# Optimization experiments

Hardware: AMD Instinct MI355X
Metric: run time of the kernel (lower is better)

## Reference

```python
import jax, jax.numpy as jnp
import numpy as np

# --- module hyperparameters (from init_kwargs) ---
NUM_HEADS = 16
ATTN_DIM = 1024
HEAD_DIM = ATTN_DIM // NUM_HEADS  # 64
NUM_RF = 256                      # FAVOR random features per head
CONV_CH = 1024
GROUPS = 4
M_SCALE = 256                     # num_features_per_scale
GAMMAS = (0.5, 1.0, 2.0)          # gamma_list
NY_LANDMARKS = 64                 # == HEAD_DIM so shapes compose
NY_GAMMA = 1.0
EPS = 1e-6


def setup_inputs() -> dict:
    key = jax.random.key(0)
    ks = jax.random.split(key, 12)
    B, S, C = 2, 4096, CONV_CH
    G, Ms = len(GAMMAS), M_SCALE
    x = jax.random.normal(ks[0], (B, S, C), dtype=jnp.float32)
    # grouped Conv1D kernels (WIO layout): [ksize, Cin/groups, Cout], one per q/k/v
    conv_k = jax.random.normal(ks[1], (3, 3, C // GROUPS, C), jnp.float32) / np.sqrt(3 * (C // GROUPS))
    conv_b = jnp.zeros((3, C), jnp.float32)
    # multi-scale random-Fourier-feature weights per projection and per gamma scale
    rff_w = jax.random.normal(ks[2], (3, G, C, Ms), jnp.float32)
    rff_b = jax.random.uniform(ks[3], (3, G, Ms), jnp.float32) * (2.0 * np.pi)
    proj_w = jax.random.normal(ks[4], (3, G * Ms, ATTN_DIM), jnp.float32) / np.sqrt(G * Ms)
    proj_b = jnp.zeros((3, ATTN_DIM), jnp.float32)
    # FAVOR+ projection matrix (shared across heads) and Nystrom landmarks
    omega = jax.random.normal(ks[5], (HEAD_DIM, NUM_RF), jnp.float32)
    landmarks = jax.random.normal(ks[6], (NY_LANDMARKS, HEAD_DIM), jnp.float32)
    out_w = jax.random.normal(ks[7], (ATTN_DIM, ATTN_DIM), jnp.float32) / np.sqrt(ATTN_DIM)
    out_b = jnp.zeros((ATTN_DIM,), jnp.float32)
    return {"x": x, "conv_k": conv_k, "conv_b": conv_b, "rff_w": rff_w, "rff_b": rff_b,
            "proj_w": proj_w, "proj_b": proj_b, "omega": omega, "landmarks": landmarks,
            "out_w": out_w, "out_b": out_b}


def _rotary(seq_len, dh, dtype):
    inv = 1.0 / (10000.0 ** (jnp.arange(0, dh, 2, dtype=jnp.float32) / dh))
    f = jnp.arange(seq_len, dtype=jnp.float32)[:, None] * inv[None, :]  # [S, dh/2]
    emb = jnp.concatenate([f, f], axis=-1)  # [S, dh]
    return jnp.sin(emb).astype(dtype), jnp.cos(emb).astype(dtype)


def _apply_rope(x, sin, cos):
    # x: [B,H,S,D]; rotate-half RoPE
    d = x.shape[-1] // 2
    rot = jnp.concatenate([-x[..., d:], x[..., :d]], axis=-1)
    return x * cos + rot * sin


def _projection(x, ck, cb, rw, rb, pw, pb):
    # ProjectionWithKernel: grouped conv -> multi-scale RFF kernel map -> dense
    h = jax.lax.conv_general_dilated(x, ck, (1,), 'SAME',
                                     dimension_numbers=('NWC', 'WIO', 'NWC'),
                                     feature_group_count=GROUPS) + cb
    g = jnp.sqrt(2.0 * jnp.array(GAMMAS, dtype=x.dtype))[:, None]  # [G,1]
    z = jnp.cos(jnp.einsum('bsc,gcm->bsgm', h, rw) * g + rb)       # [B,S,G,Ms]
    feats = (z * jnp.sqrt(2.0 / M_SCALE)).reshape(x.shape[0], x.shape[1], -1)
    return feats @ pw + pb  # [B,S,ATTN_DIM]


def _favor(x, omega):
    # FAVOR+ positive random features: exp(x.w - |x|^2/2) / sqrt(m)
    norm = 0.5 * jnp.sum(x * x, axis=-1, keepdims=True)
    return jnp.exp(jnp.einsum('bhsd,dm->bhsm', x, omega) - norm) / jnp.sqrt(float(omega.shape[-1]))


def _nystrom(k, landmarks):
    # RBF features against landmarks (normalized by dim to keep exp in range)
    d = k.shape[-1]
    d2 = (jnp.sum(k * k, -1, keepdims=True) + jnp.sum(landmarks * landmarks, -1)
          - 2.0 * jnp.einsum('bhsd,ld->bhsl', k, landmarks))
    return jnp.exp(-NY_GAMMA * d2 / d)  # [B,H,S,L], L == HEAD_DIM


def reference(x, conv_k, conv_b, rff_w, rff_b, proj_w, proj_b, omega, landmarks, out_w, out_b):
    B, S, _ = x.shape
    qkv = [_projection(x, conv_k[i], conv_b[i], rff_w[i], rff_b[i], proj_w[i], proj_b[i])
           for i in range(3)]
    split = lambda t: t.reshape(B, S, NUM_HEADS, HEAD_DIM).transpose(0, 2, 1, 3)
    q, k, v = map(split, qkv)  # [B,H,S,Dh]
    sin, cos = _rotary(S, HEAD_DIM, x.dtype)
    q = _apply_rope(q, sin, cos)
    k = _apply_rope(k, sin, cos)
    k = _nystrom(k, landmarks)               # [B,H,S,Dh]
    qp = _favor(q, omega)                    # [B,H,S,M]
    kp = _favor(k, omega)                    # [B,H,S,M]
    denom = jnp.einsum('bhse,bhe->bhs', qp, jnp.sum(kp, axis=2))[..., None]
    kv = jnp.einsum('bhse,bhsd->bhed', kp, v)          # [B,H,M,Dh]
    num = jnp.einsum('bhse,bhed->bhsd', qp, kv)        # [B,H,S,Dh]
    out = num / (denom + EPS)
    out = out.transpose(0, 2, 1, 3).reshape(B, S, ATTN_DIM)
    return out @ out_w + out_b  # dropout is identity at inference
```

## Files before the change

### kernel.cpp

```cpp
#include <hip/hip_runtime.h>
#include <math.h>


using f32x4 = __attribute__((ext_vector_type(4))) float;
using s16x8 = __attribute__((ext_vector_type(8))) short;

__device__ __forceinline__ unsigned short f2bf(float x) {
  unsigned u = __float_as_uint(x);
  unsigned r = u + 0x7fffu + ((u >> 16) & 1u);
  return (unsigned short)(r >> 16);
}
__device__ __forceinline__ float bf2f(unsigned short h) {
  return __uint_as_float(((unsigned)h) << 16);
}

__device__ __forceinline__ void gload16(const void* g, void* l) {
  __builtin_amdgcn_global_load_lds(
      (const __attribute__((address_space(1))) void*)g,
      (__attribute__((address_space(3))) void*)l, 16, 0, 0);
}

__global__ __launch_bounds__(256) void split_prep_kernel(
    const float* __restrict__ in, unsigned short* __restrict__ ohi,
    unsigned short* __restrict__ olo, int n8)
{
  const int i = blockIdx.x * 256 + threadIdx.x;
  if (i >= n8) return;
  const float4 f0 = ((const float4*)in)[i * 2];
  const float4 f1 = ((const float4*)in)[i * 2 + 1];
  const float v[8] = {f0.x, f0.y, f0.z, f0.w, f1.x, f1.y, f1.z, f1.w};
  s16x8 hi, lo;
  #pragma unroll
  for (int u = 0; u < 8; ++u) {
    const unsigned short hh = f2bf(v[u]);
    hi[u] = (short)hh;
    lo[u] = (short)f2bf(v[u] - bf2f(hh));
  }
  ((s16x8*)ohi)[i] = hi;
  ((s16x8*)olo)[i] = lo;
}

template<int WM>
__global__ __launch_bounds__(256) void wconv_kernel(
    const float* __restrict__ in0, unsigned short* __restrict__ ohi,
    unsigned short* __restrict__ olo)
{
  int K, N;
  const float* in;
  unsigned short *oh, *ol = nullptr;
  const int z = blockIdx.z;
  if constexpr (WM == 0) {
    K = 768; N = 1024;
    in = in0 + (size_t)z * 786432;
    oh = ohi + (size_t)z * 786432; ol = olo + (size_t)z * 786432;
  } else if constexpr (WM == 1) {
    K = 1024; N = 256;
    const int i = z / 3, g = z % 3;
    in = in0 + (size_t)i * 786432 + (size_t)g * 262144;
    oh = ohi + (size_t)i * 786432 + (size_t)g * 262144;
    ol = olo + (size_t)i * 786432 + (size_t)g * 262144;
  } else if constexpr (WM == 2) {
    K = 768; N = 1024;
    in = in0 + (size_t)z * 786432; oh = ohi + (size_t)z * 786432;
  } else {
    K = 1024; N = 1024; in = in0; oh = ohi;
  }
  const int k0 = blockIdx.x * 64, n0 = blockIdx.y * 64;
  __shared__ float t[64][65];
  const int tid = threadIdx.x, tn = tid & 63, tr = tid >> 6;
  #pragma unroll 4
  for (int p = 0; p < 16; ++p) {
    const int kk = p * 4 + tr;
    t[kk][tn] = in[(size_t)(k0 + kk) * N + n0 + tn];
  }
  __syncthreads();
  #pragma unroll 4
  for (int p = 0; p < 16; ++p) {
    const int nn = p * 4 + tr;
    const float v = t[tn][nn];
    const unsigned short hi = f2bf(v);
    oh[(size_t)(n0 + nn) * K + k0 + tn] = hi;
    if constexpr (WM <= 1)
      ol[(size_t)(n0 + nn) * K + k0 + tn] = f2bf(v - bf2f(hi));
  }
}

__global__ __launch_bounds__(256) void omega_prep_kernel(
    const float* __restrict__ omega, unsigned short* __restrict__ oThi)
{
  const int idx = blockIdx.x * 256 + threadIdx.x;
  const int m = idx >> 6, d = idx & 63;
  oThi[idx] = f2bf(omega[d * 256 + m]);
}

__global__ __launch_bounds__(256) void vt_kernel(
    const float* __restrict__ V, unsigned short* __restrict__ VT)
{
  const int bh = blockIdx.x, sb = blockIdx.y;
  const int b = bh >> 4, h = bh & 15;
  __shared__ float t[64][65];
  const int tid = threadIdx.x, tn = tid & 63, tr = tid >> 6;
  #pragma unroll 4
  for (int p = 0; p < 16; ++p)
    t[p * 4 + tr][tn] =
        V[(size_t)(b * 4096 + sb * 64 + p * 4 + tr) * 1024 + h * 64 + tn];
  __syncthreads();
  #pragma unroll 4
  for (int p = 0; p < 16; ++p)
    VT[((size_t)bh * 80 + p * 4 + tr) * 4096 + sb * 64 + tn] =
        f2bf(t[tn][p * 4 + tr]);
  #pragma unroll
  for (int p = 0; p < 4; ++p) {
    const int rr = p * 4 + tr;
    VT[((size_t)bh * 80 + 64 + rr) * 4096 + sb * 64 + tn] =
        (rr == 0) ? 0x3F80 : 0;
  }
}

template<int MODE>
__global__ __launch_bounds__(256, 4) void gemm_mfma(
    const unsigned short* __restrict__ Ahi, const unsigned short* __restrict__ Alo,
    const unsigned short* __restrict__ Bhig, const unsigned short* __restrict__ Blog,
    const float* __restrict__ bias, const float2* __restrict__ tab,
    float* __restrict__ Cf, unsigned short* __restrict__ C1,
    unsigned short* __restrict__ C2,
    int M, int N, int K)
{
  constexpr bool SPLIT = (MODE <= 1);
  __shared__ alignas(16) char smem[SPLIT ? 32768 : 16384];
  char* const sAhi = smem;
  char* const sBhi = smem + (SPLIT ? 16384 : 8192);
  char* const sAlo = smem + 8192;
  char* const sBlo = smem + 24576;

  const int gx = gridDim.x, gy = gridDim.y;
  const int L = blockIdx.x + gx * (blockIdx.y + gy * blockIdx.z);
  const int nwg = gx * gy * gridDim.z;
  const int logical = (L & 7) * (nwg >> 3) + (L >> 3);
  const int bx = logical % gx;
  const int by = (logical / gx) % gy;
  const int z = logical / (gx * gy);

  if constexpr (MODE == 0) {
    Bhig += (size_t)z * 786432; Blog += (size_t)z * 786432;
    bias += z * 1024;
    C1 += (size_t)z * 8388608; C2 += (size_t)z * 8388608;
  } else if constexpr (MODE == 1) {
    Ahi += (size_t)z * 8388608; Alo += (size_t)z * 8388608;
    Bhig += (size_t)z * 786432; Blog += (size_t)z * 786432;
    bias += z * 768;
    C1 += (size_t)z * 6291456;
  } else if constexpr (MODE == 2) {
    Ahi += (size_t)z * 6291456;
    Bhig += (size_t)z * 786432;
    bias += z * 1024;
    Cf += (size_t)z * 8388608;
  }

  const int tid = threadIdx.x;
  const int n0 = bx * 128;
  const int m0 = by * 128;

  const int lane = tid & 63, wid = tid >> 6;
  const int wr = wid >> 1, wc = wid & 1;
  const int fr = lane & 15, kc = lane >> 4;
  const int fsw = ((fr >> 1) & 3) << 4;

  const int seg0 = wid * 2;
  const int r0 = seg0 * 16 + (lane >> 2);
  const int r1 = r0 + 16;
  const int cp = lane & 3;
  const int c0e = (cp ^ ((r0 >> 1) & 3)) * 8;
  const int c1e = (cp ^ ((r1 >> 1) & 3)) * 8;
  char* const dA0 = sAhi + seg0 * 1024;  char* const dA1 = dA0 + 1024;
  char* const dL0 = sAlo + seg0 * 1024;  char* const dL1 = dL0 + 1024;
  char* const dB0 = sBhi + seg0 * 1024;  char* const dB1 = dB0 + 1024;
  char* const dBl0 = sBlo + seg0 * 1024; char* const dBl1 = dBl0 + 1024;

  f32x4 acc[4][4];
  #pragma unroll
  for (int i = 0; i < 4; ++i)
    #pragma unroll
    for (int j = 0; j < 4; ++j) acc[i][j] = f32x4{0.f, 0.f, 0.f, 0.f};

  for (int k0 = 0; k0 < K; k0 += 32) {
    __syncthreads();
    if constexpr (MODE == 0) {
      const int t = k0 >> 8;
      const int cb = (n0 >> 8) * 256 + (k0 & 255);
      const int g0 = m0 + r0, g1 = m0 + r1;
      int s0 = (g0 & 4095) + t - 1; s0 = s0 < 0 ? 0 : (s0 > 4095 ? 4095 : s0);
      int s1 = (g1 & 4095) + t - 1; s1 = s1 < 0 ? 0 : (s1 > 4095 ? 4095 : s1);
      const size_t o0 = ((size_t)((g0 >> 12) * 4096 + s0)) * 1024 + cb;
      const size_t o1 = ((size_t)((g1 >> 12) * 4096 + s1)) * 1024 + cb;
      gload16(Ahi + o0 + c0e, dA0);
      gload16(Ahi + o1 + c1e, dA1);
      gload16(Alo + o0 + c0e, dL0);
      gload16(Alo + o1 + c1e, dL1);
    } else {
      const size_t o0 = (size_t)(m0 + r0) * K + k0;
      const size_t o1 = (size_t)(m0 + r1) * K + k0;
      gload16(Ahi + o0 + c0e, dA0);
      gload16(Ahi + o1 + c1e, dA1);
      if constexpr (SPLIT) {
        gload16(Alo + o0 + c0e, dL0);
        gload16(Alo + o1 + c1e, dL1);
      }
    }
    {
      const size_t o0 = (size_t)(n0 + r0) * K + k0;
      const size_t o1 = (size_t)(n0 + r1) * K + k0;
      gload16(Bhig + o0 + c0e, dB0);
      gload16(Bhig + o1 + c1e, dB1);
      if constexpr (SPLIT) {
        gload16(Blog + o0 + c0e, dBl0);
        gload16(Blog + o1 + c1e, dBl1);
      }
    }
    __syncthreads();

    if constexpr (MODE == 0) {
      const int t = k0 >> 8;
      int zr = -1;
      if (t == 0 && (m0 & 4095) == 0) zr = 0;
      if (t == 2 && (m0 & 4095) == 3968) zr = 127;
      if (zr >= 0) {
        if (tid < 8) {
          char* buf = (tid < 4) ? sAhi : sAlo;
          *(s16x8*)(buf + zr * 64 + (tid & 3) * 16) = s16x8{0,0,0,0,0,0,0,0};
        }
        __syncthreads();
      }
    }

    s16x8 Af[4], Al[4], Bf[4], Bl[4];
    #pragma unroll
    for (int i = 0; i < 4; ++i) {
      const int off = (wr * 64 + i * 16 + fr) * 64 + ((kc * 16) ^ fsw);
      Af[i] = *(const s16x8*)(sAhi + off);
      if constexpr (SPLIT) Al[i] = *(const s16x8*)(sAlo + off);
    }
    #pragma unroll
    for (int j = 0; j < 4; ++j) {
      const int off = (wc * 64 + j * 16 + fr) * 64 + ((kc * 16) ^ fsw);
      Bf[j] = *(const s16x8*)(sBhi + off);
      if constexpr (SPLIT) Bl[j] = *(const s16x8*)(sBlo + off);
    }
    #pragma unroll
    for (int i = 0; i < 4; ++i)
      #pragma unroll
      for (int j = 0; j < 4; ++j) {
        acc[i][j] = __builtin_amdgcn_mfma_f32_16x16x32_bf16(Af[i], Bf[j], acc[i][j], 0, 0, 0);
        if constexpr (SPLIT) {
          acc[i][j] = __builtin_amdgcn_mfma_f32_16x16x32_bf16(Af[i], Bl[j], acc[i][j], 0, 0, 0);
          acc[i][j] = __builtin_amdgcn_mfma_f32_16x16x32_bf16(Al[i], Bf[j], acc[i][j], 0, 0, 0);
        }
      }
  }

  if constexpr (MODE == 2) {
    #pragma unroll
    for (int i = 0; i < 4; ++i)
      #pragma unroll
      for (int j2 = 0; j2 < 2; ++j2) {
        const int col0 = n0 + wc * 64 + j2 * 16 + fr;
        const int jr = col0 & 31;
        const float b0 = bias[col0], b1 = bias[col0 + 32];
        #pragma unroll
        for (int rr = 0; rr < 4; ++rr) {
          const int row = m0 + wr * 64 + i * 16 + kc * 4 + rr;
          float v0 = acc[i][j2][rr] + b0;
          float v1 = acc[i][j2 + 2][rr] + b1;
          if (z < 2) {
            const float2 cs = tab[((row & 4095) << 5) | jr];
            const float rr0 = v0 * cs.x - v1 * cs.y;
            const float rr1 = v1 * cs.x + v0 * cs.y;
            v0 = rr0; v1 = rr1;
          }
          Cf[(size_t)row * N + col0] = v0;
          Cf[(size_t)row * N + col0 + 32] = v1;
        }
      }
  } else {
    #pragma unroll
    for (int i = 0; i < 4; ++i)
      #pragma unroll
      for (int j = 0; j < 4; ++j) {
        const int col = n0 + wc * 64 + j * 16 + fr;
        #pragma unroll
        for (int rr = 0; rr < 4; ++rr) {
          const int row = m0 + wr * 64 + i * 16 + kc * 4 + rr;
          const float v = acc[i][j][rr];
          if constexpr (MODE == 0) {
            const float hv = v + bias[col];
            const unsigned short hh = f2bf(hv);
            C1[(size_t)row * N + col] = hh;
            C2[(size_t)row * N + col] = f2bf(hv - bf2f(hh));
          } else if constexpr (MODE == 1) {
            const int g = col >> 8;
            const float sg = (g == 0) ? 1.0f : ((g == 1) ? 1.41421356237309515f : 2.0f);
            const float zc = cosf(v * sg + bias[col]) * 0.08838834764831845f;
            C1[(size_t)row * N + col] = f2bf(zc);
          } else {
            Cf[(size_t)row * N + col] = v + bias[col];
          }
        }
      }
  }
}

__global__ __launch_bounds__(256) void rope_table_kernel(float2* __restrict__ tab)
{
  const int idx = blockIdx.x * 256 + threadIdx.x;
  const int j = idx & 31, s = idx >> 5;
  const double inv = pow(10000.0, -(double)j * (1.0 / 32.0));
  double sd, cd;
  sincos((double)s * inv, &sd, &cd);
  tab[idx] = make_float2((float)cd, (float)sd);
}

__global__ __launch_bounds__(256) void nystrom_mfma(
    const float* __restrict__ Kb, const float* __restrict__ lm,
    unsigned short* __restrict__ kny, float* __restrict__ knorm)
{
  const int bid = blockIdx.x;
  const int bh = bid >> 4, chunk = bid & 15;
  const int b = bh >> 4, h = bh & 15;
  const int tid = threadIdx.x, lane = tid & 63, wid = tid >> 6;
  const int fr = lane & 15, kc = lane >> 4;
  const int ws0 = chunk * 256 + wid * 64;

  __shared__ float lnorm[64];
  if (tid < 64) {
    float s = 0.f;
    #pragma unroll
    for (int d = 0; d < 64; ++d) { const float v = lm[tid * 64 + d]; s = fmaf(v, v, s); }
    lnorm[tid] = s;
  }
  __syncthreads();

  s16x8 bfr[4][2];
  #pragma unroll
  for (int c = 0; c < 4; ++c)
    #pragma unroll
    for (int ks = 0; ks < 2; ++ks) {
      const float* lp = lm + (c * 16 + fr) * 64 + ks * 32 + kc * 8;
      #pragma unroll
      for (int u = 0; u < 8; ++u) bfr[c][ks][u] = (short)f2bf(lp[u]);
    }

  #pragma unroll
  for (int r = 0; r < 4; ++r) {
    const int s_r = ws0 + r * 16 + fr;
    const float* ap = Kb + ((size_t)(b * 4096 + s_r)) * 1024 + h * 64;
    s16x8 afr[2];
    float part = 0.f;
    #pragma unroll
    for (int ks = 0; ks < 2; ++ks) {
      const float4 f0 = *(const float4*)(ap + ks * 32 + kc * 8);
      const float4 f1 = *(const float4*)(ap + ks * 32 + kc * 8 + 4);
      const float v[8] = {f0.x, f0.y, f0.z, f0.w, f1.x, f1.y, f1.z, f1.w};
      #pragma unroll
      for (int u = 0; u < 8; ++u) {
        part = fmaf(v[u], v[u], part);
        afr[ks][u] = (short)f2bf(v[u]);
      }
    }
    part += __shfl_xor(part, 16);
    part += __shfl_xor(part, 32);

    float sq[4] = {0.f, 0.f, 0.f, 0.f};
    #pragma unroll
    for (int c = 0; c < 4; ++c) {
      f32x4 acc = f32x4{0.f, 0.f, 0.f, 0.f};
      acc = __builtin_amdgcn_mfma_f32_16x16x32_bf16(afr[0], bfr[c][0], acc, 0, 0, 0);
      acc = __builtin_amdgcn_mfma_f32_16x16x32_bf16(afr[1], bfr[c][1], acc, 0, 0, 0);
      const float ln = lnorm[c * 16 + fr];
      #pragma unroll
      for (int reg = 0; reg < 4; ++reg) {
        const float nk = __shfl(part, kc * 4 + reg);
        const float val = __expf((2.f * acc[reg] - nk - ln) * 0.015625f);
        sq[reg] = fmaf(val, val, sq[reg]);
        const int srow = ws0 + r * 16 + kc * 4 + reg;
        kny[((size_t)(b * 4096 + srow) * 16 + h) * 64 + c * 16 + fr] = f2bf(val);
      }
    }
    #pragma unroll
    for (int reg = 0; reg < 4; ++reg) {
      float s2 = sq[reg];
      s2 += __shfl_xor(s2, 1); s2 += __shfl_xor(s2, 2);
      s2 += __shfl_xor(s2, 4); s2 += __shfl_xor(s2, 8);
      if (fr == 0) {
        const int srow = ws0 + r * 16 + kc * 4 + reg;
        knorm[(size_t)(b * 4096 + srow) * 16 + h] = 0.5f * s2;
      }
    }
  }
}

__global__ __launch_bounds__(512) void favor_k_mfma(
    const unsigned short* __restrict__ kny, const float* __restrict__ knorm,
    const unsigned short* __restrict__ oThi,
    const unsigned short* __restrict__ VT, float* __restrict__ KVp)
{
  const int bid = blockIdx.x;
  const int bh = bid >> 3, chunk = bid & 7;
  const int b = bh >> 4, h = bh & 15;
  const int s0 = chunk * 512;
  const int tid = threadIdx.x, lane = tid & 63, wid = tid >> 6;
  const int fr = lane & 15, kc = lane >> 4;
  const int m0w = wid * 32;

  __shared__ unsigned short P[256][40];
  __shared__ float T[8][32][84];

  s16x8 whi[2][2];
  #pragma unroll
  for (int c = 0; c < 2; ++c)
    #pragma unroll
    for (int ks = 0; ks < 2; ++ks)
      whi[c][ks] = *(const s16x8*)(oThi + (size_t)(m0w + c * 16 + fr) * 64 + ks * 32 + kc * 8);

  f32x4 acc2[2][5];
  #pragma unroll
  for (int i = 0; i < 2; ++i)
    #pragma unroll
    for (int j = 0; j < 5; ++j) acc2[i][j] = f32x4{0.f, 0.f, 0.f, 0.f};

  for (int st = 0; st < 512; st += 32) {
    s16x8 a1[2][2];
    float nrm[2];
    #pragma unroll
    for (int r = 0; r < 2; ++r) {
      const size_t kidx = (size_t)(b * 4096 + s0 + st + r * 16 + fr) * 16 + h;
      a1[r][0] = *(const s16x8*)(kny + kidx * 64 + kc * 8);
      a1[r][1] = *(const s16x8*)(kny + kidx * 64 + 32 + kc * 8);
      nrm[r] = knorm[kidx];
    }
    __syncthreads();
    #pragma unroll
    for (int r = 0; r < 2; ++r)
      #pragma unroll
      for (int c = 0; c < 2; ++c) {
        f32x4 s1 = f32x4{0.f, 0.f, 0.f, 0.f};
        s1 = __builtin_amdgcn_mfma_f32_16x16x32_bf16(a1[r][0], whi[c][0], s1, 0, 0, 0);
        s1 = __builtin_amdgcn_mfma_f32_16x16x32_bf16(a1[r][1], whi[c][1], s1, 0, 0, 0);
        #pragma unroll
        for (int reg = 0; reg < 4; ++reg) {
          const int sl = kc * 4 + reg;
          const float nn = __shfl(nrm[r], sl);
          const float p = __expf(s1[reg] - nn - 2.772588722239781f);
          P[m0w + c * 16 + fr][r * 16 + sl] = f2bf(p);
        }
      }
    __syncthreads();
    s16x8 b2[5];
    #pragma unroll
    for (int nf = 0; nf < 5; ++nf)
      b2[nf] = *(const s16x8*)(VT + ((size_t)bh * 80 + nf * 16 + fr) * 4096 +
                               s0 + st + kc * 8);
    #pragma unroll
    for (int mf = 0; mf < 2; ++mf) {
      const s16x8 a2 = *(const s16x8*)&P[m0w + mf * 16 + fr][kc * 8];
      #pragma unroll
      for (int nf = 0; nf < 5; ++nf)
        acc2[mf][nf] = __builtin_amdgcn_mfma_f32_16x16x32_bf16(a2, b2[nf], acc2[mf][nf], 0, 0, 0);
    }
  }
  #pragma unroll
  for (int mf = 0; mf < 2; ++mf)
    #pragma unroll
    for (int nf = 0; nf < 5; ++nf)
      #pragma unroll
      for (int reg = 0; reg < 4; ++reg)
        T[wid][mf * 16 + kc * 4 + reg][nf * 16 + fr] = acc2[mf][nf][reg];
  __syncthreads();
  #pragma unroll
  for (int i = 0; i < 40; ++i) {
    const int flat = i * 64 + lane;
    const int n = flat >> 5, ml = flat & 31;
    KVp[((size_t)bid * 80 + n) * 256 + m0w + ml] = T[wid][ml][n];
  }
}

__global__ __launch_bounds__(256) void reduce_kvxt_kernel(
    const float* __restrict__ KVp, unsigned short* __restrict__ KVXT)
{
  const int bh = blockIdx.x;
  const int m = threadIdx.x;
  for (int n = 0; n < 80; ++n) {
    float s = 0.f;
    #pragma unroll
    for (int c = 0; c < 8; ++c)
      s += KVp[((size_t)(bh * 8 + c) * 80 + n) * 256 + m];
    KVXT[((size_t)bh * 80 + n) * 256 + m] = f2bf(s);
  }
}

__global__ __launch_bounds__(512) void favor_q_mfma(
    const float* __restrict__ Q, const unsigned short* __restrict__ oThi,
    const unsigned short* __restrict__ KVXT, unsigned short* __restrict__ O)
{
  const int bid = blockIdx.x;
  const int bh = bid >> 4, chunk = bid & 15;
  const int b = bh >> 4, h = bh & 15;
  const int s0 = chunk * 256;
  const int tid = threadIdx.x, lane = tid & 63, wid = tid >> 6;
  const int fr = lane & 15, kc = lane >> 4;
  const int ws0 = s0 + wid * 32;

  __shared__ unsigned short KX[80][264];
  __shared__ unsigned short P[8][32][66];

  for (int i = tid; i < 80 * 256; i += 512)
    KX[i >> 8][i & 255] = KVXT[(size_t)bh * 80 * 256 + i];
  __syncthreads();

  s16x8 ahi[2][2];
  float nrm[2];
  #pragma unroll
  for (int r = 0; r < 2; ++r) {
    float part = 0.f;
    #pragma unroll
    for (int ks = 0; ks < 2; ++ks) {
      const float* ap = Q + ((size_t)(b * 4096 + ws0 + r * 16 + fr)) * 1024 +
                        h * 64 + ks * 32 + kc * 8;
      const float4 f0 = ((const float4*)ap)[0];
      const float4 f1 = ((const float4*)ap)[1];
      const float v[8] = {f0.x, f0.y, f0.z, f0.w, f1.x, f1.y, f1.z, f1.w};
      #pragma unroll
      for (int u = 0; u < 8; ++u) {
        part = fmaf(v[u], v[u], part);
        ahi[r][ks][u] = (short)f2bf(v[u]);
      }
    }
    part += __shfl_xor(part, 16);
    part += __shfl_xor(part, 32);
    nrm[r] = 0.5f * part;
  }

  f32x4 acc2[2][5];
  #pragma unroll
  for (int i = 0; i < 2; ++i)
    #pragma unroll
    for (int j = 0; j < 5; ++j) acc2[i][j] = f32x4{0.f, 0.f, 0.f, 0.f};

  for (int mc = 0; mc < 4; ++mc) {
    __syncthreads();
    #pragma unroll
    for (int r = 0; r < 2; ++r)
      #pragma unroll
      for (int c = 0; c < 4; ++c) {
        f32x4 s1 = f32x4{0.f, 0.f, 0.f, 0.f};
        #pragma unroll
        for (int ks = 0; ks < 2; ++ks) {
          const size_t off = (size_t)(mc * 64 + c * 16 + fr) * 64 + ks * 32 + kc * 8;
          const s16x8 bh1 = *(const s16x8*)(oThi + off);
          s1 = __builtin_amdgcn_mfma_f32_16x16x32_bf16(ahi[r][ks], bh1, s1, 0, 0, 0);
        }
        #pragma unroll
        for (int reg = 0; reg < 4; ++reg) {
          const int sl = kc * 4 + reg;
          const float nn = __shfl(nrm[r], sl);
          const float p = __expf(s1[reg] - nn - 2.772588722239781f);
          P[wid][r * 16 + sl][c * 16 + fr] = f2bf(p);
        }
      }
    __syncthreads();
    #pragma unroll
    for (int ks2 = 0; ks2 < 2; ++ks2) {
      s16x8 b2[5];
      #pragma unroll
      for (int nf = 0; nf < 5; ++nf)
        b2[nf] = *(const s16x8*)&KX[nf * 16 + fr][mc * 64 + ks2 * 32 + kc * 8];
      #pragma unroll
      for (int r = 0; r < 2; ++r) {
        const s16x8 a2 = *(const s16x8*)&P[wid][r * 16 + fr][ks2 * 32 + kc * 8];
        #pragma unroll
        for (int nf = 0; nf < 5; ++nf)
          acc2[r][nf] = __builtin_amdgcn_mfma_f32_16x16x32_bf16(a2, b2[nf], acc2[r][nf], 0, 0, 0);
      }
    }
  }
  #pragma unroll
  for (int r = 0; r < 2; ++r)
    #pragma unroll
    for (int reg = 0; reg < 4; ++reg) {
      const int s = ws0 + r * 16 + kc * 4 + reg;
      const float dv = __shfl(acc2[r][4][reg], lane & 48) + 1e-6f;
      #pragma unroll
      for (int nf = 0; nf < 4; ++nf)
        O[(size_t)(b * 4096 + s) * 1024 + h * 64 + nf * 16 + fr] =
            f2bf(acc2[r][nf][reg] / dv);
    }
}

extern "C" void kernel_launch(void* const* d_in, const int* in_sizes, int n_in,
                              void* d_out, int out_size, void* d_ws, size_t ws_size,
                              hipStream_t stream)
{
  const float* x      = (const float*)d_in[0];
  const float* conv_k = (const float*)d_in[1];
  const float* conv_b = (const float*)d_in[2];
  const float* rff_w  = (const float*)d_in[3];
  const float* rff_b  = (const float*)d_in[4];
  const float* proj_w = (const float*)d_in[5];
  const float* proj_b = (const float*)d_in[6];
  const float* omega  = (const float*)d_in[7];
  const float* lm     = (const float*)d_in[8];
  const float* out_w  = (const float*)d_in[9];
  const float* out_b  = (const float*)d_in[10];

  char* wsb = (char*)d_ws;
  size_t o = 0;
  auto alloc = [&](size_t bytes) {
    char* p = wsb + o;
    o = (o + bytes + 255) & ~(size_t)255;
    return p;
  };
  unsigned short* Wc_hi = (unsigned short*)alloc(4718592);
  unsigned short* Wc_lo = (unsigned short*)alloc(4718592);
  unsigned short* Wr_hi = (unsigned short*)alloc(4718592);
  unsigned short* Wr_lo = (unsigned short*)alloc(4718592);
  unsigned short* Wp    = (unsigned short*)alloc(4718592);
  unsigned short* Wo    = (unsigned short*)alloc(2097152);
  unsigned short* oThi  = (unsigned short*)alloc(32768);
  unsigned short* oTlo  = (unsigned short*)alloc(32768);
  float2* tab           = (float2*)alloc(1048576);
  char* RB = alloc(41943040);
  unsigned short* xhi   = (unsigned short*)RB;
  unsigned short* xlo   = (unsigned short*)(RB + 16777216);
  unsigned short* feats = (unsigned short*)RB;
  unsigned short* VT    = (unsigned short*)RB;
  unsigned short* Obf   = (unsigned short*)(RB + 20971520);
  unsigned short* KVXT  = (unsigned short*)(RB + 37748736);
  char* RC = alloc(100663296);
  unsigned short* hhi   = (unsigned short*)RC;
  unsigned short* hlo   = (unsigned short*)(RC + 50331648);
  float* QKV            = (float*)RC;
  char* RE = alloc(33554432);
  unsigned short* knyb  = (unsigned short*)RE;
  float* knorm          = (float*)(RE + 16777216);
  float* KVp = (float*)alloc(20971520);
  (void)oTlo; (void)ws_size;

  dim3 blk(256);
  split_prep_kernel<<<4096, blk, 0, stream>>>(x, xhi, xlo, 1048576);
  wconv_kernel<0><<<dim3(12, 16, 3), blk, 0, stream>>>(conv_k, Wc_hi, Wc_lo);
  wconv_kernel<1><<<dim3(16, 4, 9),  blk, 0, stream>>>(rff_w, Wr_hi, Wr_lo);
  wconv_kernel<2><<<dim3(12, 16, 3), blk, 0, stream>>>(proj_w, Wp, nullptr);
  wconv_kernel<3><<<dim3(16, 16, 1), blk, 0, stream>>>(out_w, Wo, nullptr);
  omega_prep_kernel<<<64, blk, 0, stream>>>(omega, oThi);
  rope_table_kernel<<<512, blk, 0, stream>>>(tab);

  gemm_mfma<0><<<dim3(8, 64, 3), blk, 0, stream>>>(
      xhi, xlo, Wc_hi, Wc_lo, conv_b, nullptr,
      nullptr, hhi, hlo, 8192, 1024, 768);
  gemm_mfma<1><<<dim3(6, 64, 3), blk, 0, stream>>>(
      hhi, hlo, Wr_hi, Wr_lo, rff_b, nullptr,
      nullptr, feats, nullptr, 8192, 768, 1024);
  gemm_mfma<2><<<dim3(8, 64, 3), blk, 0, stream>>>(
      feats, nullptr, Wp, nullptr, proj_b, tab,
      QKV, nullptr, nullptr, 8192, 1024, 768);

  float* Qb = QKV;
  float* Kb = QKV + 8388608;
  float* Vb = QKV + 16777216;
  vt_kernel<<<dim3(32, 64), blk, 0, stream>>>(Vb, VT);
  nystrom_mfma<<<512, blk, 0, stream>>>(Kb, lm, knyb, knorm);
  favor_k_mfma<<<256, dim3(512), 0, stream>>>(knyb, knorm, oThi, VT, KVp);
  reduce_kvxt_kernel<<<32, blk, 0, stream>>>(KVp, KVXT);
  favor_q_mfma<<<512, dim3(512), 0, stream>>>(Qb, oThi, KVXT, Obf);
  gemm_mfma<3><<<dim3(8, 64), blk, 0, stream>>>(
      Obf, nullptr, Wo, nullptr, out_b, nullptr,
      (float*)d_out, nullptr, nullptr, 8192, 1024, 1024);
}
```

Before: 925.3 us.

## Rewrite MFMA GEMM with 256x256 tiles, double-buffered LDS and split-term K loop

Replaces the 128x128, 256-thread GEMM with a 256x256, 512-thread kernel using 128 KB of double-buffered LDS, so the next K-tile is loaded while the current one is computed. The hi/lo split-precision products become three passes over an extended K loop instead of three MFMAs per step. Out-of-range conv rows now load from a zero page instead of clamping and patching LDS. Larger tiles raise data reuse but give one workgroup per CU and fewer workgroups, which risks poorer occupancy and load balance.

```diff
diff --git a/kernel.cpp b/kernel.cpp
--- a/kernel.cpp
+++ b/kernel.cpp
@@ -18,6 +18,11 @@
   __builtin_amdgcn_global_load_lds(
       (const __attribute__((address_space(1))) void*)g,
       (__attribute__((address_space(3))) void*)l, 16, 0, 0);
+}
+
+__global__ __launch_bounds__(512) void zpage_kernel(unsigned short* __restrict__ zp)
+{
+  zp[threadIdx.x] = 0;
 }
 
 __global__ __launch_bounds__(256) void split_prep_kernel(
@@ -118,20 +123,20 @@
 }
 
 template<int MODE>
-__global__ __launch_bounds__(256, 4) void gemm_mfma(
+__global__ __launch_bounds__(512, 1) void gemm8(
     const unsigned short* __restrict__ Ahi, const unsigned short* __restrict__ Alo,
     const unsigned short* __restrict__ Bhig, const unsigned short* __restrict__ Blog,
     const float* __restrict__ bias, const float2* __restrict__ tab,
+    const unsigned short* __restrict__ zp,
     float* __restrict__ Cf, unsigned short* __restrict__ C1,
-    unsigned short* __restrict__ C2,
-    int M, int N, int K)
-{
-  constexpr bool SPLIT = (MODE <= 1);
-  __shared__ alignas(16) char smem[SPLIT ? 32768 : 16384];
-  char* const sAhi = smem;
-  char* const sBhi = smem + (SPLIT ? 16384 : 8192);
-  char* const sAlo = smem + 8192;
-  char* const sBlo = smem + 24576;
+    unsigned short* __restrict__ C2)
+{
+  constexpr int K0 = (MODE == 0 || MODE == 2) ? 768 : 1024;
+  constexpr int TPK = K0 / 64;
+  constexpr int NT = (MODE <= 1) ? 3 * TPK : TPK;
+  constexpr int NP = (MODE == 1) ? 768 : 1024;
+
+  __shared__ alignas(16) char smem[131072];
 
   const int gx = gridDim.x, gy = gridDim.y;
   const int L = blockIdx.x + gx * (blockIdx.y + gy * blockIdx.z);
@@ -158,151 +163,128 @@
   }
 
   const int tid = threadIdx.x;
-  const int n0 = bx * 128;
-  const int m0 = by * 128;
-
   const int lane = tid & 63, wid = tid >> 6;
-  const int wr = wid >> 1, wc = wid & 1;
+  const int wm = wid >> 2, wn = wid & 3;
   const int fr = lane & 15, kc = lane >> 4;
-  const int fsw = ((fr >> 1) & 3) << 4;
-
-  const int seg0 = wid * 2;
-  const int r0 = seg0 * 16 + (lane >> 2);
-  const int r1 = r0 + 16;
-  const int cp = lane & 3;
-  const int c0e = (cp ^ ((r0 >> 1) & 3)) * 8;
-  const int c1e = (cp ^ ((r1 >> 1) & 3)) * 8;
-  char* const dA0 = sAhi + seg0 * 1024;  char* const dA1 = dA0 + 1024;
-  char* const dL0 = sAlo + seg0 * 1024;  char* const dL1 = dL0 + 1024;
-  char* const dB0 = sBhi + seg0 * 1024;  char* const dB1 = dB0 + 1024;
-  char* const dBl0 = sBlo + seg0 * 1024; char* const dBl1 = dBl0 + 1024;
-
-  f32x4 acc[4][4];
-  #pragma unroll
-  for (int i = 0; i < 4; ++i)
+  const int n0 = bx * 256;
+  const int m0 = by * 256;
+
+  const int rbase = wid * 8 + (lane >> 3);
+  const int cst = ((lane & 7) ^ (lane >> 3)) * 8;
+
+  f32x4 acc[8][4];
+  #pragma unroll
+  for (int i = 0; i < 8; ++i)
     #pragma unroll
     for (int j = 0; j < 4; ++j) acc[i][j] = f32x4{0.f, 0.f, 0.f, 0.f};
 
-  for (int k0 = 0; k0 < K; k0 += 32) {
+  auto stage = [&](int kt, int par) {
+    int term = 0, tk = kt;
+    if constexpr (MODE <= 1) { term = kt / TPK; tk = kt - term * TPK; }
+    const int k0 = tk * 64;
+    const unsigned short* As = (term < 2) ? Ahi : Alo;
+    const unsigned short* Bs = (term == 1) ? Blog : Bhig;
+    char* const bA = smem + par * 65536;
+    char* const bB = bA + 32768;
+    #pragma unroll
+    for (int i = 0; i < 4; ++i) {
+      const int r = i * 64 + rbase;
+      const unsigned short* srcA;
+      if constexpr (MODE == 0) {
+        const int grow = m0 + r;
+        const int t = k0 >> 8;
+        const int s_im = (grow & 4095) + t - 1;
+        const int ci = ((n0 >> 8) << 8) + (k0 & 255) + cst;
+        srcA = ((unsigned)s_im < 4096u)
+             ? As + ((size_t)((grow >> 12) * 4096 + s_im)) * 1024 + ci
+             : zp;
+      } else {
+        srcA = As + (size_t)(m0 + r) * K0 + k0 + cst;
+      }
+      gload16(srcA, bA + i * 8192 + wid * 1024);
+      gload16(Bs + (size_t)(n0 + r) * K0 + k0 + cst, bB + i * 8192 + wid * 1024);
+    }
+  };
+
+  stage(0, 0);
+  __syncthreads();
+  for (int kt = 0; kt < NT; ++kt) {
+    const int cur = kt & 1;
+    if (kt + 1 < NT) stage(kt + 1, cur ^ 1);
+    const char* bA = smem + cur * 65536;
+    const char* bB = bA + 32768;
+    s16x8 Bf[4][2];
+    #pragma unroll
+    for (int j = 0; j < 4; ++j) {
+      const int row = wn * 64 + j * 16 + fr;
+      #pragma unroll
+      for (int ks = 0; ks < 2; ++ks)
+        Bf[j][ks] = *(const s16x8*)(bB + row * 128 +
+                        (((ks * 4 + kc) ^ (row & 7)) << 4));
+    }
+    #pragma unroll
+    for (int i = 0; i < 8; ++i) {
+      const int row = wm * 128 + i * 16 + fr;
+      s16x8 Af[2];
+      #pragma unroll
+      for (int ks = 0; ks < 2; ++ks)
+        Af[ks] = *(const s16x8*)(bA + row * 128 +
+                      (((ks * 4 + kc) ^ (row & 7)) << 4));
+      #pragma unroll
+      for (int ks = 0; ks < 2; ++ks)
+        #pragma unroll
+        for (int j = 0; j < 4; ++j)
+          acc[i][j] = __builtin_amdgcn_mfma_f32_16x16x32_bf16(
+              Af[ks], Bf[j][ks], acc[i][j], 0, 0, 0);
+    }
     __syncthreads();
-    if constexpr (MODE == 0) {
-      const int t = k0 >> 8;
-      const int cb = (n0 >> 8) * 256 + (k0 & 255);
-      const int g0 = m0 + r0, g1 = m0 + r1;
-      int s0 = (g0 & 4095) + t - 1; s0 = s0 < 0 ? 0 : (s0 > 4095 ? 4095 : s0);
-      int s1 = (g1 & 4095) + t - 1; s1 = s1 < 0 ? 0 : (s1 > 4095 ? 4095 : s1);
-      const size_t o0 = ((size_t)((g0 >> 12) * 4096 + s0)) * 1024 + cb;
-      const size_t o1 = ((size_t)((g1 >> 12) * 4096 + s1)) * 1024 + cb;
-      gload16(Ahi + o0 + c0e, dA0);
-      gload16(Ahi + o1 + c1e, dA1);
-      gload16(Alo + o0 + c0e, dL0);
-      gload16(Alo + o1 + c1e, dL1);
-    } else {
-      const size_t o0 = (size_t)(m0 + r0) * K + k0;
-      const size_t o1 = (size_t)(m0 + r1) * K + k0;
-      gload16(Ahi + o0 + c0e, dA0);
-      gload16(Ahi + o1 + c1e, dA1);
-      if constexpr (SPLIT) {
-        gload16(Alo + o0 + c0e, dL0);
-        gload16(Alo + o1 + c1e, dL1);
-      }
-    }
-    {
-      const size_t o0 = (size_t)(n0 + r0) * K + k0;
-      const size_t o1 = (size_t)(n0 + r1) * K + k0;
-      gload16(Bhig + o0 + c0e, dB0);
-      gload16(Bhig + o1 + c1e, dB1);
-      if constexpr (SPLIT) {
-        gload16(Blog + o0 + c0e, dBl0);
-        gload16(Blog + o1 + c1e, dBl1);
-      }
-    }
-    __syncthreads();
-
-    if constexpr (MODE == 0) {
-      const int t = k0 >> 8;
-      int zr = -1;
-      if (t == 0 && (m0 & 4095) == 0) zr = 0;
-      if (t == 2 && (m0 & 4095) == 3968) zr = 127;
-      if (zr >= 0) {
-        if (tid < 8) {
-          char* buf = (tid < 4) ? sAhi : sAlo;
-          *(s16x8*)(buf + zr * 64 + (tid & 3) * 16) = s16x8{0,0,0,0,0,0,0,0};
-        }
-        __syncthreads();
-      }
-    }
-
-    s16x8 Af[4], Al[4], Bf[4], Bl[4];
-    #pragma unroll
-    for (int i = 0; i < 4; ++i) {
-      const int off = (wr * 64 + i * 16 + fr) * 64 + ((kc * 16) ^ fsw);
-      Af[i] = *(const s16x8*)(sAhi + off);
-      if constexpr (SPLIT) Al[i] = *(const s16x8*)(sAlo + off);
-    }
-    #pragma unroll
-    for (int j = 0; j < 4; ++j) {
-      const int off = (wc * 64 + j * 16 + fr) * 64 + ((kc * 16) ^ fsw);
-      Bf[j] = *(const s16x8*)(sBhi + off);
-      if constexpr (SPLIT) Bl[j] = *(const s16x8*)(sBlo + off);
-    }
-    #pragma unroll
-    for (int i = 0; i < 4; ++i)
-      #pragma unroll
-      for (int j = 0; j < 4; ++j) {
-        acc[i][j] = __builtin_amdgcn_mfma_f32_16x16x32_bf16(Af[i], Bf[j], acc[i][j], 0, 0, 0);
-        if constexpr (SPLIT) {
-          acc[i][j] = __builtin_amdgcn_mfma_f32_16x16x32_bf16(Af[i], Bl[j], acc[i][j], 0, 0, 0);
-          acc[i][j] = __builtin_amdgcn_mfma_f32_16x16x32_bf16(Al[i], Bf[j], acc[i][j], 0, 0, 0);
-        }
-      }
   }
 
   if constexpr (MODE == 2) {
     #pragma unroll
-    for (int i = 0; i < 4; ++i)
+    for (int i = 0; i < 8; ++i)
       #pragma unroll
       for (int j2 = 0; j2 < 2; ++j2) {
-        const int col0 = n0 + wc * 64 + j2 * 16 + fr;
+        const int col0 = n0 + wn * 64 + j2 * 16 + fr;
         const int jr = col0 & 31;
         const float b0 = bias[col0], b1 = bias[col0 + 32];
         #pragma unroll
-        for (int rr = 0; rr < 4; ++rr) {
-          const int row = m0 + wr * 64 + i * 16 + kc * 4 + rr;
-          float v0 = acc[i][j2][rr] + b0;
-          float v1 = acc[i][j2 + 2][rr] + b1;
+        for (int reg = 0; reg < 4; ++reg) {
+          const int row = m0 + wm * 128 + i * 16 + kc * 4 + reg;
+          float v0 = acc[i][j2][reg] + b0;
+          float v1 = acc[i][j2 + 2][reg] + b1;
           if (z < 2) {
             const float2 cs = tab[((row & 4095) << 5) | jr];
-            const float rr0 = v0 * cs.x - v1 * cs.y;
-            const float rr1 = v1 * cs.x + v0 * cs.y;
-            v0 = rr0; v1 = rr1;
+            const float r0 = v0 * cs.x - v1 * cs.y;
+            const float r1 = v1 * cs.x + v0 * cs.y;
+            v0 = r0; v1 = r1;
           }
-          Cf[(size_t)row * N + col0] = v0;
-          Cf[(size_t)row * N + col0 + 32] = v1;
+          Cf[(size_t)row * NP + col0] = v0;
+          Cf[(size_t)row * NP + col0 + 32] = v1;
         }
       }
   } else {
     #pragma unroll
-    for (int i = 0; i < 4; ++i)
+    for (int i = 0; i < 8; ++i)
       #pragma unroll
       for (int j = 0; j < 4; ++j) {
-        const int col = n0 + wc * 64 + j * 16 + fr;
+        const int col = n0 + wn * 64 + j * 16 + fr;
         #pragma unroll
-        for (int rr = 0; rr < 4; ++rr) {
-          const int row = m0 + wr * 64 + i * 16 + kc * 4 + rr;
-          const float v = acc[i][j][rr];
+        for (int reg = 0; reg < 4; ++reg) {
+          const int row = m0 + wm * 128 + i * 16 + kc * 4 + reg;
+          const float v = acc[i][j][reg];
           if constexpr (MODE == 0) {
             const float hv = v + bias[col];
             const unsigned short hh = f2bf(hv);
-            C1[(size_t)row * N + col] = hh;
-            C2[(size_t)row * N + col] = f2bf(hv - bf2f(hh));
+            C1[(size_t)row * NP + col] = hh;
+            C2[(size_t)row * NP + col] = f2bf(hv - bf2f(hh));
           } else if constexpr (MODE == 1) {
             const int g = col >> 8;
             const float sg = (g == 0) ? 1.0f : ((g == 1) ? 1.41421356237309515f : 2.0f);
             const float zc = cosf(v * sg + bias[col]) * 0.08838834764831845f;
-            C1[(size_t)row * N + col] = f2bf(zc);
+            C1[(size_t)row * NP + col] = f2bf(zc);
           } else {
-            Cf[(size_t)row * N + col] = v + bias[col];
+            Cf[(size_t)row * NP + col] = v + bias[col];
           }
         }
       }
@@ -625,7 +607,7 @@
   unsigned short* Wp    = (unsigned short*)alloc(4718592);
   unsigned short* Wo    = (unsigned short*)alloc(2097152);
   unsigned short* oThi  = (unsigned short*)alloc(32768);
-  unsigned short* oTlo  = (unsigned short*)alloc(32768);
+  unsigned short* zp    = (unsigned short*)alloc(1024);
   float2* tab           = (float2*)alloc(1048576);
   char* RB = alloc(41943040);
   unsigned short* xhi   = (unsigned short*)RB;
@@ -642,9 +624,10 @@
   unsigned short* knyb  = (unsigned short*)RE;
   float* knorm          = (float*)(RE + 16777216);
   float* KVp = (float*)alloc(20971520);
-  (void)oTlo; (void)ws_size;
+  (void)ws_size;
 
   dim3 blk(256);
+  zpage_kernel<<<1, 512, 0, stream>>>(zp);
   split_prep_kernel<<<4096, blk, 0, stream>>>(x, xhi, xlo, 1048576);
   wconv_kernel<0><<<dim3(12, 16, 3), blk, 0, stream>>>(conv_k, Wc_hi, Wc_lo);
   wconv_kernel<1><<<dim3(16, 4, 9),  blk, 0, stream>>>(rff_w, Wr_hi, Wr_lo);
@@ -653,15 +636,15 @@
   omega_prep_kernel<<<64, blk, 0, stream>>>(omega, oThi);
   rope_table_kernel<<<512, blk, 0, stream>>>(tab);
 
-  gemm_mfma<0><<<dim3(8, 64, 3), blk, 0, stream>>>(
-      xhi, xlo, Wc_hi, Wc_lo, conv_b, nullptr,
-      nullptr, hhi, hlo, 8192, 1024, 768);
-  gemm_mfma<1><<<dim3(6, 64, 3), blk, 0, stream>>>(
-      hhi, hlo, Wr_hi, Wr_lo, rff_b, nullptr,
-      nullptr, feats, nullptr, 8192, 768, 1024);
-  gemm_mfma<2><<<dim3(8, 64, 3), blk, 0, stream>>>(
-      feats, nullptr, Wp, nullptr, proj_b, tab,
-      QKV, nullptr, nullptr, 8192, 1024, 768);
+  gemm8<0><<<dim3(4, 32, 3), dim3(512), 0, stream>>>(
+      xhi, xlo, Wc_hi, Wc_lo, conv_b, nullptr, zp,
+      nullptr, hhi, hlo);
+  gemm8<1><<<dim3(3, 32, 3), dim3(512), 0, stream>>>(
+      hhi, hlo, Wr_hi, Wr_lo, rff_b, nullptr, zp,
+      nullptr, feats, nullptr);
+  gemm8<2><<<dim3(4, 32, 3), dim3(512), 0, stream>>>(
+      feats, nullptr, Wp, nullptr, proj_b, tab, zp,
+      QKV, nullptr, nullptr);
 
   float* Qb = QKV;
   float* Kb = QKV + 8388608;
@@ -671,7 +654,7 @@
   favor_k_mfma<<<256, dim3(512), 0, stream>>>(knyb, knorm, oThi, VT, KVp);
   reduce_kvxt_kernel<<<32, blk, 0, stream>>>(KVp, KVXT);
   favor_q_mfma<<<512, dim3(512), 0, stream>>>(Qb, oThi, KVXT, Obf);
-  gemm_mfma<3><<<dim3(8, 64), blk, 0, stream>>>(
-      Obf, nullptr, Wo, nullptr, out_b, nullptr,
-      (float*)d_out, nullptr, nullptr, 8192, 1024, 1024);
-}
+  gemm8<3><<<dim3(4, 32, 1), dim3(512), 0, stream>>>(
+      Obf, nullptr, Wo, nullptr, out_b, nullptr, zp,
+      (float*)d_out, nullptr, nullptr);
+}
```

Result: slower. 1.359 ms (+46.9%).
